# Kernel tuning notes

Hardware: AMD Instinct MI355X
Metric: run time of the kernel (lower is better)

The kernel has to match this reference:

```python
import jax, jax.numpy as jnp
import numpy as np

E = 262144   # total child->parent edges (flattened mailboxes)
N = 32768    # number of parent nodes
H = 256      # h_size == x_size


def setup_inputs() -> dict:
    key = jax.random.key(0)
    ks = jax.random.split(key, 9)
    s = 1.0 / np.sqrt(H)
    child_h = jax.random.normal(ks[0], (E, H), dtype=jnp.float32)
    child_c = jax.random.normal(ks[1], (E, H), dtype=jnp.float32)
    x = jax.random.normal(ks[2], (N, H), dtype=jnp.float32)
    parent_idx = jnp.sort(jax.random.randint(ks[3], (E,), 0, N))
    # learned parameters (torch nn.Linear convention: y = x @ W.T + b)
    U_iou_w = jax.random.uniform(ks[4], (3 * H, H), minval=-s, maxval=s, dtype=jnp.float32)
    b_iou = jnp.zeros((1, 3 * H), dtype=jnp.float32)
    U_f_w = jax.random.uniform(ks[5], (H, H), minval=-s, maxval=s, dtype=jnp.float32)
    W_f_w = jax.random.uniform(ks[6], (H, H), minval=-s, maxval=s, dtype=jnp.float32)
    W_f_b = jax.random.uniform(ks[7], (H,), minval=-s, maxval=s, dtype=jnp.float32)
    return {"child_h": child_h, "child_c": child_c, "x": x, "parent_idx": parent_idx,
            "U_iou_w": U_iou_w, "b_iou": b_iou, "U_f_w": U_f_w, "W_f_w": W_f_w, "W_f_b": W_f_b}


def reference(child_h, child_c, x, parent_idx, U_iou_w, b_iou, U_f_w, W_f_w, W_f_b):
    n = x.shape[0]
    # forget gate per edge: sigmoid(U_f h_j + W_f x_parent + b)
    wf_x = x @ W_f_w.T + W_f_b                      # [N, H], computed once per node
    f = jax.nn.sigmoid(child_h @ U_f_w.T + wf_x[parent_idx])   # [E, H]
    # child-sum aggregation (reduce_func)
    c_agg = jax.ops.segment_sum(f * child_c, parent_idx, num_segments=n,
                                indices_are_sorted=True)        # [N, H]
    h_sum = jax.ops.segment_sum(child_h, parent_idx, num_segments=n,
                                indices_are_sorted=True)        # [N, H]
    # apply_node_func
    iou = h_sum @ U_iou_w.T + b_iou                 # [N, 3H]
    i, o, u = jnp.split(iou, 3, axis=1)
    c = jax.nn.sigmoid(i) * jnp.tanh(u) + c_agg
    h = jax.nn.sigmoid(o) * jnp.tanh(c)
    return h, c
```

## Files before the change

kernel.cpp:

```cpp
#include <hip/hip_runtime.h>

#define E_EDGES 262144
#define N_NODES 32768
#define HDIM 256

typedef __bf16 bf16;
typedef __attribute__((ext_vector_type(8))) __bf16 bf16x8;
typedef __attribute__((ext_vector_type(4))) __bf16 bf16x4;
typedef __attribute__((ext_vector_type(4))) float f32x4;
typedef __attribute__((ext_vector_type(4))) int i32x4;

__device__ __forceinline__ float sigm(float z) { return 1.0f / (1.0f + __expf(-z)); }
__device__ __forceinline__ float tanh_(float z) { return 1.0f - 2.0f / (1.0f + __expf(2.0f * z)); }

__device__ __forceinline__ void stage_tile(const float* __restrict__ src, char* lds) {
  const int t = threadIdx.x;
  const int rsub = t >> 4, l16 = t & 15;
#pragma unroll
  for (int it = 0; it < 4; ++it) {
    const int row = it * 16 + rsub;
    const float4* p = (const float4*)(src + (size_t)row * HDIM);
#pragma unroll
    for (int j = 0; j < 4; ++j) {
      float4 v = p[j * 16 + l16];
      unsigned byte = (unsigned)(row * 512 + (j * 16 + l16) * 8);
      byte ^= (unsigned)((row & 7) << 4);
      bf16x4 w;
      w.x = (bf16)v.x; w.y = (bf16)v.y; w.z = (bf16)v.z; w.w = (bf16)v.w;
      *(bf16x4*)(lds + byte) = w;
    }
  }
}

__device__ __forceinline__ void stage_chunk(const bf16* __restrict__ w, int kc, char* lds) {
  const int t = threadIdx.x;
  const i32x4* src = (const i32x4*)(w + (size_t)t * HDIM + kc * 32);
  i32x4* dst = (i32x4*)(lds + t * 80);
#pragma unroll
  for (int j = 0; j < 4; ++j) dst[j] = src[j];
}

__device__ __forceinline__ void mfma_kc(const char* ldsA, const char* ldsB, int kc,
                                        f32x4 (&acc)[4][4]) {
  const int l = threadIdx.x & 63, w = threadIdx.x >> 6;
  const int c16 = l & 15, rg = l >> 4;
  bf16x8 a[4], b[4];
#pragma unroll
  for (int ai = 0; ai < 4; ++ai) {
    const int row = ai * 16 + c16;
    unsigned byte = (unsigned)(row * 512 + kc * 64 + (rg << 4));
    byte ^= (unsigned)((row & 7) << 4);
    a[ai] = *(const bf16x8*)(ldsA + byte);
  }
#pragma unroll
  for (int bj = 0; bj < 4; ++bj) {
    const int wrow = w * 64 + bj * 16 + c16;
    b[bj] = *(const bf16x8*)(ldsB + wrow * 80 + (rg << 4));
  }
#pragma unroll
  for (int ai = 0; ai < 4; ++ai)
#pragma unroll
    for (int bj = 0; bj < 4; ++bj)
      acc[ai][bj] = __builtin_amdgcn_mfma_f32_16x16x32_bf16(a[ai], b[bj], acc[ai][bj], 0, 0, 0);
}

__device__ __forceinline__ void scan_cols(const char* ldsA, const int* pl,
                                          float* __restrict__ dst) {
  const int t = threadIdx.x;
  if (t < 128) {
    float a0 = 0.f, a1 = 0.f;
#pragma unroll 8
    for (int r = 0; r < 64; ++r) {
      unsigned byte = (unsigned)(r * 512 + t * 4) ^ (unsigned)((r & 7) << 4);
      unsigned v = *(const unsigned*)(ldsA + byte);
      a0 += __uint_as_float(v << 16);
      a1 += __uint_as_float(v & 0xffff0000u);
      if (pl[r + 1] != pl[r]) {
        float* d = dst + (size_t)pl[r] * HDIM + t * 2;
        atomicAdd(d, a0);
        atomicAdd(d + 1, a1);
        a0 = 0.f; a1 = 0.f;
      }
    }
  }
}

__global__ __launch_bounds__(256) void cvt_weights(
    const float* __restrict__ uf, const float* __restrict__ wf,
    const float* __restrict__ uiou, bf16* __restrict__ ufb, bf16* __restrict__ wfb,
    bf16* __restrict__ uioub) {
  const int i = blockIdx.x * 256 + threadIdx.x;
  ufb[i] = (bf16)uf[i];
  wfb[i] = (bf16)wf[i];
#pragma unroll
  for (int j = 0; j < 3; ++j) uioub[i + j * 65536] = (bf16)uiou[i + j * 65536];
}

__global__ __launch_bounds__(256) void wfx_kernel(const float* __restrict__ x,
                                                  const bf16* __restrict__ wfb,
                                                  const float* __restrict__ wfbias,
                                                  bf16* __restrict__ wfx) {
  __shared__ char ldsA[32768];
  __shared__ char ldsB[20480];
  const int m0 = blockIdx.x * 64;
  stage_tile(x + (size_t)m0 * HDIM, ldsA);
  f32x4 acc[4][4];
#pragma unroll
  for (int ai = 0; ai < 4; ++ai)
#pragma unroll
    for (int bj = 0; bj < 4; ++bj) acc[ai][bj] = (f32x4){0.f, 0.f, 0.f, 0.f};
  for (int kc = 0; kc < 8; ++kc) {
    __syncthreads();
    stage_chunk(wfb, kc, ldsB);
    __syncthreads();
    mfma_kc(ldsA, ldsB, kc, acc);
  }
  const int l = threadIdx.x & 63, w = threadIdx.x >> 6;
  const int c16 = l & 15, rg = l >> 4;
#pragma unroll
  for (int ai = 0; ai < 4; ++ai)
#pragma unroll
    for (int bj = 0; bj < 4; ++bj) {
      const int col = w * 64 + bj * 16 + c16;
      const float bias = wfbias[col];
#pragma unroll
      for (int r = 0; r < 4; ++r) {
        const int row = m0 + ai * 16 + rg * 4 + r;
        wfx[(size_t)row * HDIM + col] = (bf16)(acc[ai][bj][r] + bias);
      }
    }
}

__global__ __launch_bounds__(256) void edge_kernel(
    const float* __restrict__ child_h, const float* __restrict__ child_c,
    const int* __restrict__ parent, const bf16* __restrict__ ufb,
    const bf16* __restrict__ wfx, float* __restrict__ h_sum,
    float* __restrict__ c_agg) {
  __shared__ char ldsA[32768];
  __shared__ char ldsB[20480];
  __shared__ int pl[65];
  const int bid = (int)blockIdx.x;
  const int blk = (bid & 7) * (E_EDGES / 64 / 8) + (bid >> 3);
  const int e0 = blk * 64;
  const int t = threadIdx.x;
  if (t < 64) pl[t] = parent[e0 + t];
  if (t == 64) pl[64] = -1;
  stage_tile(child_h + (size_t)e0 * HDIM, ldsA);
  __syncthreads();
  stage_chunk(ufb, 0, ldsB);
  scan_cols(ldsA, pl, h_sum);
  __syncthreads();
  f32x4 acc[4][4];
#pragma unroll
  for (int ai = 0; ai < 4; ++ai)
#pragma unroll
    for (int bj = 0; bj < 4; ++bj) acc[ai][bj] = (f32x4){0.f, 0.f, 0.f, 0.f};
  mfma_kc(ldsA, ldsB, 0, acc);
  for (int kc = 1; kc < 8; ++kc) {
    __syncthreads();
    stage_chunk(ufb, kc, ldsB);
    __syncthreads();
    mfma_kc(ldsA, ldsB, kc, acc);
  }
  __syncthreads();
  const int l = t & 63, w = t >> 6;
  const int c16 = l & 15, rg = l >> 4;
#pragma unroll
  for (int ai = 0; ai < 4; ++ai)
#pragma unroll
    for (int bj = 0; bj < 4; ++bj) {
      const int col = w * 64 + bj * 16 + c16;
#pragma unroll
      for (int r = 0; r < 4; ++r) {
        const int row = ai * 16 + rg * 4 + r;
        const int p = pl[row];
        float z = acc[ai][bj][r] + (float)wfx[(size_t)p * HDIM + col];
        float f = sigm(z);
        float fc = f * child_c[(size_t)(e0 + row) * HDIM + col];
        unsigned byte = (unsigned)(row * 512 + col * 2) ^ (unsigned)((row & 7) << 4);
        *(bf16*)(ldsA + byte) = (bf16)fc;
      }
    }
  __syncthreads();
  scan_cols(ldsA, pl, c_agg);
}

__global__ __launch_bounds__(256) void node_kernel(const float* __restrict__ h_sum,
                                                   const float* __restrict__ c_agg,
                                                   const bf16* __restrict__ uioub,
                                                   const float* __restrict__ b_iou,
                                                   float* __restrict__ out) {
  __shared__ char ldsA[32768];
  __shared__ char ldsB[20480];
  const int m0 = blockIdx.x * 64;
  stage_tile(h_sum + (size_t)m0 * HDIM, ldsA);
  const int l = threadIdx.x & 63, w = threadIdx.x >> 6;
  const int c16 = l & 15, rg = l >> 4;
  f32x4 uacc[4][4], acc[4][4];
#pragma unroll
  for (int ai = 0; ai < 4; ++ai)
#pragma unroll
    for (int bj = 0; bj < 4; ++bj) uacc[ai][bj] = (f32x4){0.f, 0.f, 0.f, 0.f};
  for (int kc = 0; kc < 8; ++kc) {
    __syncthreads();
    stage_chunk(uioub + 2 * 65536, kc, ldsB);
    __syncthreads();
    mfma_kc(ldsA, ldsB, kc, uacc);
  }
#pragma unroll
  for (int ai = 0; ai < 4; ++ai)
#pragma unroll
    for (int bj = 0; bj < 4; ++bj) {
      const float bu = b_iou[512 + w * 64 + bj * 16 + c16];
#pragma unroll
      for (int r = 0; r < 4; ++r) uacc[ai][bj][r] += bu;
    }
#pragma unroll
  for (int ai = 0; ai < 4; ++ai)
#pragma unroll
    for (int bj = 0; bj < 4; ++bj) acc[ai][bj] = (f32x4){0.f, 0.f, 0.f, 0.f};
  for (int kc = 0; kc < 8; ++kc) {
    __syncthreads();
    stage_chunk(uioub, kc, ldsB);
    __syncthreads();
    mfma_kc(ldsA, ldsB, kc, acc);
  }
#pragma unroll
  for (int ai = 0; ai < 4; ++ai)
#pragma unroll
    for (int bj = 0; bj < 4; ++bj) {
      const int col = w * 64 + bj * 16 + c16;
      const float bi = b_iou[col];
#pragma unroll
      for (int r = 0; r < 4; ++r) {
        const int row = m0 + ai * 16 + rg * 4 + r;
        float cc = sigm(acc[ai][bj][r] + bi) * tanh_(uacc[ai][bj][r]) +
                   c_agg[(size_t)row * HDIM + col];
        out[(size_t)N_NODES * HDIM + (size_t)row * HDIM + col] = cc;
        uacc[ai][bj][r] = cc;
      }
    }
#pragma unroll
  for (int ai = 0; ai < 4; ++ai)
#pragma unroll
    for (int bj = 0; bj < 4; ++bj) acc[ai][bj] = (f32x4){0.f, 0.f, 0.f, 0.f};
  for (int kc = 0; kc < 8; ++kc) {
    __syncthreads();
    stage_chunk(uioub + 65536, kc, ldsB);
    __syncthreads();
    mfma_kc(ldsA, ldsB, kc, acc);
  }
#pragma unroll
  for (int ai = 0; ai < 4; ++ai)
#pragma unroll
    for (int bj = 0; bj < 4; ++bj) {
      const int col = w * 64 + bj * 16 + c16;
      const float bo = b_iou[256 + col];
#pragma unroll
      for (int r = 0; r < 4; ++r) {
        const int row = m0 + ai * 16 + rg * 4 + r;
        out[(size_t)row * HDIM + col] = sigm(acc[ai][bj][r] + bo) * tanh_(uacc[ai][bj][r]);
      }
    }
}

extern "C" void kernel_launch(void* const* d_in, const int* in_sizes, int n_in,
                              void* d_out, int out_size, void* d_ws, size_t ws_size,
                              hipStream_t stream) {
  const float* child_h = (const float*)d_in[0];
  const float* child_c = (const float*)d_in[1];
  const float* x       = (const float*)d_in[2];
  const int*   parent  = (const int*)d_in[3];
  const float* U_iou_w = (const float*)d_in[4];
  const float* b_iou   = (const float*)d_in[5];
  const float* U_f_w   = (const float*)d_in[6];
  const float* W_f_w   = (const float*)d_in[7];
  const float* W_f_b   = (const float*)d_in[8];
  float* out = (float*)d_out;

  char* ws = (char*)d_ws;
  float* h_sum = (float*)ws;
  float* c_agg = h_sum + (size_t)N_NODES * HDIM;
  bf16* wfxb   = (bf16*)(c_agg + (size_t)N_NODES * HDIM);
  bf16* ufb    = wfxb + (size_t)N_NODES * HDIM;
  bf16* wfb    = ufb + 65536;
  bf16* uioub  = wfb + 65536;

  hipMemsetAsync(h_sum, 0, (size_t)2 * N_NODES * HDIM * sizeof(float), stream);
  cvt_weights<<<256, 256, 0, stream>>>(U_f_w, W_f_w, U_iou_w, ufb, wfb, uioub);
  wfx_kernel<<<N_NODES / 64, 256, 0, stream>>>(x, wfb, W_f_b, wfxb);
  edge_kernel<<<E_EDGES / 64, 256, 0, stream>>>(child_h, child_c, parent, ufb, wfxb,
                                                h_sum, c_agg);
  node_kernel<<<N_NODES / 64, 256, 0, stream>>>(h_sum, c_agg, uioub, b_iou, out);
}
```

Measured before the change: 1.024 ms.

## Keep weight B-fragments in registers and loop edge tiles per block

Weight fragments are now loaded once straight from global memory into 32 registers per thread, which removes the per-k-chunk LDS staging of weights and its paired barriers. The edge kernel becomes persistent, with 1024 blocks each processing 4 consecutive 64-edge tiles, so the register-held U_f weights are reused across tiles. The node kernel keeps the tanh(u) and tanh(c) intermediates in a 64KB LDS buffer instead of a second accumulator array, which lowers register pressure. The trade-off is a large register footprint under launch_bounds(256,2), fewer blocks in the edge grid, and extra LDS use in the node kernel, all of which can reduce occupancy.

```diff
diff --git a/kernel.cpp b/kernel.cpp
--- a/kernel.cpp
+++ b/kernel.cpp
@@ -8,7 +8,6 @@
 typedef __attribute__((ext_vector_type(8))) __bf16 bf16x8;
 typedef __attribute__((ext_vector_type(4))) __bf16 bf16x4;
 typedef __attribute__((ext_vector_type(4))) float f32x4;
-typedef __attribute__((ext_vector_type(4))) int i32x4;
 
 __device__ __forceinline__ float sigm(float z) { return 1.0f / (1.0f + __expf(-z)); }
 __device__ __forceinline__ float tanh_(float z) { return 1.0f - 2.0f / (1.0f + __expf(2.0f * z)); }
@@ -32,36 +31,41 @@
   }
 }
 
-__device__ __forceinline__ void stage_chunk(const bf16* __restrict__ w, int kc, char* lds) {
-  const int t = threadIdx.x;
-  const i32x4* src = (const i32x4*)(w + (size_t)t * HDIM + kc * 32);
-  i32x4* dst = (i32x4*)(lds + t * 80);
-#pragma unroll
-  for (int j = 0; j < 4; ++j) dst[j] = src[j];
-}
-
-__device__ __forceinline__ void mfma_kc(const char* ldsA, const char* ldsB, int kc,
-                                        f32x4 (&acc)[4][4]) {
+__device__ __forceinline__ void load_breg(const bf16* __restrict__ wsrc,
+                                          bf16x8 (&b)[32]) {
   const int l = threadIdx.x & 63, w = threadIdx.x >> 6;
   const int c16 = l & 15, rg = l >> 4;
-  bf16x8 a[4], b[4];
-#pragma unroll
-  for (int ai = 0; ai < 4; ++ai) {
-    const int row = ai * 16 + c16;
-    unsigned byte = (unsigned)(row * 512 + kc * 64 + (rg << 4));
-    byte ^= (unsigned)((row & 7) << 4);
-    a[ai] = *(const bf16x8*)(ldsA + byte);
-  }
-#pragma unroll
-  for (int bj = 0; bj < 4; ++bj) {
-    const int wrow = w * 64 + bj * 16 + c16;
-    b[bj] = *(const bf16x8*)(ldsB + wrow * 80 + (rg << 4));
-  }
-#pragma unroll
-  for (int ai = 0; ai < 4; ++ai)
-#pragma unroll
-    for (int bj = 0; bj < 4; ++bj)
-      acc[ai][bj] = __builtin_amdgcn_mfma_f32_16x16x32_bf16(a[ai], b[bj], acc[ai][bj], 0, 0, 0);
+#pragma unroll
+  for (int kc = 0; kc < 8; ++kc)
+#pragma unroll
+    for (int bj = 0; bj < 4; ++bj) {
+      const int wrow = w * 64 + bj * 16 + c16;
+      b[kc * 4 + bj] =
+          *(const bf16x8*)(wsrc + (size_t)wrow * HDIM + kc * 32 + rg * 8);
+    }
+}
+
+__device__ __forceinline__ void mfma_all(const char* ldsA, const bf16x8 (&b)[32],
+                                         f32x4 (&acc)[4][4]) {
+  const int l = threadIdx.x & 63;
+  const int c16 = l & 15, rg = l >> 4;
+#pragma unroll
+  for (int kc = 0; kc < 8; ++kc) {
+    bf16x8 a[4];
+#pragma unroll
+    for (int ai = 0; ai < 4; ++ai) {
+      const int row = ai * 16 + c16;
+      unsigned byte = (unsigned)(row * 512 + kc * 64 + (rg << 4));
+      byte ^= (unsigned)((row & 7) << 4);
+      a[ai] = *(const bf16x8*)(ldsA + byte);
+    }
+#pragma unroll
+    for (int ai = 0; ai < 4; ++ai)
+#pragma unroll
+      for (int bj = 0; bj < 4; ++bj)
+        acc[ai][bj] = __builtin_amdgcn_mfma_f32_16x16x32_bf16(a[ai], b[kc * 4 + bj],
+                                                              acc[ai][bj], 0, 0, 0);
+  }
 }
 
 __device__ __forceinline__ void scan_cols(const char* ldsA, const int* pl,
@@ -96,25 +100,22 @@
   for (int j = 0; j < 3; ++j) uioub[i + j * 65536] = (bf16)uiou[i + j * 65536];
 }
 
-__global__ __launch_bounds__(256) void wfx_kernel(const float* __restrict__ x,
-                                                  const bf16* __restrict__ wfb,
-                                                  const float* __restrict__ wfbias,
-                                                  bf16* __restrict__ wfx) {
+__global__ __launch_bounds__(256, 2) void wfx_kernel(const float* __restrict__ x,
+                                                     const bf16* __restrict__ wfb,
+                                                     const float* __restrict__ wfbias,
+                                                     bf16* __restrict__ wfx) {
   __shared__ char ldsA[32768];
-  __shared__ char ldsB[20480];
+  bf16x8 b[32];
+  load_breg(wfb, b);
   const int m0 = blockIdx.x * 64;
   stage_tile(x + (size_t)m0 * HDIM, ldsA);
+  __syncthreads();
   f32x4 acc[4][4];
 #pragma unroll
   for (int ai = 0; ai < 4; ++ai)
 #pragma unroll
     for (int bj = 0; bj < 4; ++bj) acc[ai][bj] = (f32x4){0.f, 0.f, 0.f, 0.f};
-  for (int kc = 0; kc < 8; ++kc) {
-    __syncthreads();
-    stage_chunk(wfb, kc, ldsB);
-    __syncthreads();
-    mfma_kc(ldsA, ldsB, kc, acc);
-  }
+  mfma_all(ldsA, b, acc);
   const int l = threadIdx.x & 63, w = threadIdx.x >> 6;
   const int c16 = l & 15, rg = l >> 4;
 #pragma unroll
@@ -131,100 +132,94 @@
     }
 }
 
-__global__ __launch_bounds__(256) void edge_kernel(
+__global__ __launch_bounds__(256, 2) void edge_kernel(
     const float* __restrict__ child_h, const float* __restrict__ child_c,
     const int* __restrict__ parent, const bf16* __restrict__ ufb,
     const bf16* __restrict__ wfx, float* __restrict__ h_sum,
     float* __restrict__ c_agg) {
   __shared__ char ldsA[32768];
-  __shared__ char ldsB[20480];
   __shared__ int pl[65];
+  bf16x8 b[32];
+  load_breg(ufb, b);
+  const int t = threadIdx.x;
+  const int l = t & 63, w = t >> 6;
+  const int c16 = l & 15, rg = l >> 4;
   const int bid = (int)blockIdx.x;
-  const int blk = (bid & 7) * (E_EDGES / 64 / 8) + (bid >> 3);
-  const int e0 = blk * 64;
-  const int t = threadIdx.x;
-  if (t < 64) pl[t] = parent[e0 + t];
-  if (t == 64) pl[64] = -1;
-  stage_tile(child_h + (size_t)e0 * HDIM, ldsA);
-  __syncthreads();
-  stage_chunk(ufb, 0, ldsB);
-  scan_cols(ldsA, pl, h_sum);
-  __syncthreads();
-  f32x4 acc[4][4];
-#pragma unroll
-  for (int ai = 0; ai < 4; ++ai)
-#pragma unroll
-    for (int bj = 0; bj < 4; ++bj) acc[ai][bj] = (f32x4){0.f, 0.f, 0.f, 0.f};
-  mfma_kc(ldsA, ldsB, 0, acc);
-  for (int kc = 1; kc < 8; ++kc) {
-    __syncthreads();
-    stage_chunk(ufb, kc, ldsB);
-    __syncthreads();
-    mfma_kc(ldsA, ldsB, kc, acc);
-  }
-  __syncthreads();
-  const int l = t & 63, w = t >> 6;
-  const int c16 = l & 15, rg = l >> 4;
-#pragma unroll
-  for (int ai = 0; ai < 4; ++ai)
-#pragma unroll
-    for (int bj = 0; bj < 4; ++bj) {
-      const int col = w * 64 + bj * 16 + c16;
-#pragma unroll
-      for (int r = 0; r < 4; ++r) {
-        const int row = ai * 16 + rg * 4 + r;
-        const int p = pl[row];
-        float z = acc[ai][bj][r] + (float)wfx[(size_t)p * HDIM + col];
-        float f = sigm(z);
-        float fc = f * child_c[(size_t)(e0 + row) * HDIM + col];
-        unsigned byte = (unsigned)(row * 512 + col * 2) ^ (unsigned)((row & 7) << 4);
-        *(bf16*)(ldsA + byte) = (bf16)fc;
-      }
-    }
-  __syncthreads();
-  scan_cols(ldsA, pl, c_agg);
-}
-
-__global__ __launch_bounds__(256) void node_kernel(const float* __restrict__ h_sum,
-                                                   const float* __restrict__ c_agg,
-                                                   const bf16* __restrict__ uioub,
-                                                   const float* __restrict__ b_iou,
-                                                   float* __restrict__ out) {
+  const int blk = (bid & 7) * 128 + (bid >> 3);
+#pragma unroll 1
+  for (int tt = 0; tt < 4; ++tt) {
+    const int tile = blk * 4 + tt;
+    const int e0 = tile * 64;
+    if (t < 64) pl[t] = parent[e0 + t];
+    if (t == 64) pl[64] = -1;
+    stage_tile(child_h + (size_t)e0 * HDIM, ldsA);
+    __syncthreads();
+    scan_cols(ldsA, pl, h_sum);
+    f32x4 acc[4][4];
+#pragma unroll
+    for (int ai = 0; ai < 4; ++ai)
+#pragma unroll
+      for (int bj = 0; bj < 4; ++bj) acc[ai][bj] = (f32x4){0.f, 0.f, 0.f, 0.f};
+    mfma_all(ldsA, b, acc);
+    __syncthreads();
+#pragma unroll
+    for (int ai = 0; ai < 4; ++ai)
+#pragma unroll
+      for (int bj = 0; bj < 4; ++bj) {
+        const int col = w * 64 + bj * 16 + c16;
+#pragma unroll
+        for (int r = 0; r < 4; ++r) {
+          const int row = ai * 16 + rg * 4 + r;
+          const int p = pl[row];
+          float z = acc[ai][bj][r] + (float)wfx[(size_t)p * HDIM + col];
+          float f = sigm(z);
+          float fc = f * child_c[(size_t)(e0 + row) * HDIM + col];
+          unsigned byte = (unsigned)(row * 512 + col * 2) ^ (unsigned)((row & 7) << 4);
+          *(bf16*)(ldsA + byte) = (bf16)fc;
+        }
+      }
+    __syncthreads();
+    scan_cols(ldsA, pl, c_agg);
+    __syncthreads();
+  }
+}
+
+__global__ __launch_bounds__(256, 2) void node_kernel(const float* __restrict__ h_sum,
+                                                      const float* __restrict__ c_agg,
+                                                      const bf16* __restrict__ uioub,
+                                                      const float* __restrict__ b_iou,
+                                                      float* __restrict__ out) {
   __shared__ char ldsA[32768];
-  __shared__ char ldsB[20480];
+  __shared__ float ldsU[64][256];
   const int m0 = blockIdx.x * 64;
   stage_tile(h_sum + (size_t)m0 * HDIM, ldsA);
-  const int l = threadIdx.x & 63, w = threadIdx.x >> 6;
-  const int c16 = l & 15, rg = l >> 4;
-  f32x4 uacc[4][4], acc[4][4];
-#pragma unroll
-  for (int ai = 0; ai < 4; ++ai)
-#pragma unroll
-    for (int bj = 0; bj < 4; ++bj) uacc[ai][bj] = (f32x4){0.f, 0.f, 0.f, 0.f};
-  for (int kc = 0; kc < 8; ++kc) {
-    __syncthreads();
-    stage_chunk(uioub + 2 * 65536, kc, ldsB);
-    __syncthreads();
-    mfma_kc(ldsA, ldsB, kc, uacc);
-  }
+  const int t = threadIdx.x;
+  const int l = t & 63, w = t >> 6;
+  const int c16 = l & 15, rg = l >> 4;
+  bf16x8 b[32];
+  f32x4 acc[4][4];
+  load_breg(uioub + 2 * 65536, b);
+  __syncthreads();
+#pragma unroll
+  for (int ai = 0; ai < 4; ++ai)
+#pragma unroll
+    for (int bj = 0; bj < 4; ++bj) acc[ai][bj] = (f32x4){0.f, 0.f, 0.f, 0.f};
+  mfma_all(ldsA, b, acc);
 #pragma unroll
   for (int ai = 0; ai < 4; ++ai)
 #pragma unroll
     for (int bj = 0; bj < 4; ++bj) {
       const float bu = b_iou[512 + w * 64 + bj * 16 + c16];
 #pragma unroll
-      for (int r = 0; r < 4; ++r) uacc[ai][bj][r] += bu;
-    }
-#pragma unroll
-  for (int ai = 0; ai < 4; ++ai)
-#pragma unroll
-    for (int bj = 0; bj < 4; ++bj) acc[ai][bj] = (f32x4){0.f, 0.f, 0.f, 0.f};
-  for (int kc = 0; kc < 8; ++kc) {
-    __syncthreads();
-    stage_chunk(uioub, kc, ldsB);
-    __syncthreads();
-    mfma_kc(ldsA, ldsB, kc, acc);
-  }
+      for (int r = 0; r < 4; ++r)
+        ldsU[(ai * 4 + bj) * 4 + r][t] = tanh_(acc[ai][bj][r] + bu);
+    }
+  load_breg(uioub, b);
+#pragma unroll
+  for (int ai = 0; ai < 4; ++ai)
+#pragma unroll
+    for (int bj = 0; bj < 4; ++bj) acc[ai][bj] = (f32x4){0.f, 0.f, 0.f, 0.f};
+  mfma_all(ldsA, b, acc);
 #pragma unroll
   for (int ai = 0; ai < 4; ++ai)
 #pragma unroll
@@ -234,22 +229,18 @@
 #pragma unroll
       for (int r = 0; r < 4; ++r) {
         const int row = m0 + ai * 16 + rg * 4 + r;
-        float cc = sigm(acc[ai][bj][r] + bi) * tanh_(uacc[ai][bj][r]) +
-                   c_agg[(size_t)row * HDIM + col];
+        const float tu = ldsU[(ai * 4 + bj) * 4 + r][t];
+        float cc = sigm(acc[ai][bj][r] + bi) * tu + c_agg[(size_t)row * HDIM + col];
         out[(size_t)N_NODES * HDIM + (size_t)row * HDIM + col] = cc;
-        uacc[ai][bj][r] = cc;
-      }
-    }
-#pragma unroll
-  for (int ai = 0; ai < 4; ++ai)
-#pragma unroll
-    for (int bj = 0; bj < 4; ++bj) acc[ai][bj] = (f32x4){0.f, 0.f, 0.f, 0.f};
-  for (int kc = 0; kc < 8; ++kc) {
-    __syncthreads();
-    stage_chunk(uioub + 65536, kc, ldsB);
-    __syncthreads();
-    mfma_kc(ldsA, ldsB, kc, acc);
-  }
+        ldsU[(ai * 4 + bj) * 4 + r][t] = tanh_(cc);
+      }
+    }
+  load_breg(uioub + 65536, b);
+#pragma unroll
+  for (int ai = 0; ai < 4; ++ai)
+#pragma unroll
+    for (int bj = 0; bj < 4; ++bj) acc[ai][bj] = (f32x4){0.f, 0.f, 0.f, 0.f};
+  mfma_all(ldsA, b, acc);
 #pragma unroll
   for (int ai = 0; ai < 4; ++ai)
 #pragma unroll
@@ -259,7 +250,8 @@
 #pragma unroll
       for (int r = 0; r < 4; ++r) {
         const int row = m0 + ai * 16 + rg * 4 + r;
-        out[(size_t)row * HDIM + col] = sigm(acc[ai][bj][r] + bo) * tanh_(uacc[ai][bj][r]);
+        out[(size_t)row * HDIM + col] =
+            sigm(acc[ai][bj][r] + bo) * ldsU[(ai * 4 + bj) * 4 + r][t];
       }
     }
 }
@@ -289,7 +281,7 @@
   hipMemsetAsync(h_sum, 0, (size_t)2 * N_NODES * HDIM * sizeof(float), stream);
   cvt_weights<<<256, 256, 0, stream>>>(U_f_w, W_f_w, U_iou_w, ufb, wfb, uioub);
   wfx_kernel<<<N_NODES / 64, 256, 0, stream>>>(x, wfb, W_f_b, wfxb);
-  edge_kernel<<<E_EDGES / 64, 256, 0, stream>>>(child_h, child_c, parent, ufb, wfxb,
-                                                h_sum, c_agg);
+  edge_kernel<<<1024, 256, 0, stream>>>(child_h, child_c, parent, ufb, wfxb,
+                                        h_sum, c_agg);
   node_kernel<<<N_NODES / 64, 256, 0, stream>>>(h_sum, c_agg, uioub, b_iou, out);
 }
```

New measurement: 1.239 ms. +21.0%, slower.
